# Kernel optimization log

Hardware: AMD Instinct MI355X
Metric: run time of the kernel (lower is better)

Reference implementation:

```python
import jax, jax.numpy as jnp
from jax import lax
import numpy as np

B, T, I, H, OUT = 4096, 168, 4, 64, 12


def setup_inputs() -> dict:
    key = jax.random.key(0)
    ks = jax.random.split(key, 14)
    s = 0.05
    return {
        "x": jax.random.normal(ks[0], (B, T, I), dtype=jnp.float32),
        # LSTM layer 0 (PyTorch gate order: i, f, g, o)
        "Wih0": jax.random.normal(ks[1], (4 * H, I), dtype=jnp.float32) * s,
        "Whh0": jax.random.normal(ks[2], (4 * H, H), dtype=jnp.float32) * s,
        "bih0": jax.random.normal(ks[3], (4 * H,), dtype=jnp.float32) * s,
        "bhh0": jax.random.normal(ks[4], (4 * H,), dtype=jnp.float32) * s,
        # LSTM layer 1
        "Wih1": jax.random.normal(ks[5], (4 * H, H), dtype=jnp.float32) * s,
        "Whh1": jax.random.normal(ks[6], (4 * H, H), dtype=jnp.float32) * s,
        "bih1": jax.random.normal(ks[7], (4 * H,), dtype=jnp.float32) * s,
        "bhh1": jax.random.normal(ks[8], (4 * H,), dtype=jnp.float32) * s,
        # FC head: Linear(64,64) -> ReLU -> Linear(64,12)
        "W1": jax.random.normal(ks[9], (64, H), dtype=jnp.float32) * s,
        "b1": jax.random.normal(ks[10], (64,), dtype=jnp.float32) * s,
        "W2": jax.random.normal(ks[11], (OUT, 64), dtype=jnp.float32) * s,
        "b2": jax.random.normal(ks[12], (OUT,), dtype=jnp.float32) * s,
    }


def _lstm_layer(x, Wih, Whh, bih, bhh):
    # x: [B, T, in]; returns hidden sequence [B, T, H]
    Bsz = x.shape[0]
    Hd = Whh.shape[1]
    # Precompute input contribution for all timesteps: [B, T, 4H]
    xg = jnp.einsum('bti,gi->btg', x, Wih) + bih + bhh

    def step(carry, xg_t):
        h, c = carry
        g = xg_t + h @ Whh.T  # [B, 4H]
        i, f, gg, o = jnp.split(g, 4, axis=-1)
        i = jax.nn.sigmoid(i)
        f = jax.nn.sigmoid(f)
        gg = jnp.tanh(gg)
        o = jax.nn.sigmoid(o)
        c = f * c + i * gg
        h = o * jnp.tanh(c)
        return (h, c), h

    h0 = jnp.zeros((Bsz, Hd), x.dtype)
    (_, _), hs = lax.scan(step, (h0, h0), jnp.swapaxes(xg, 0, 1))  # hs: [T, B, H]
    return jnp.swapaxes(hs, 0, 1)


def reference(x, Wih0, Whh0, bih0, bhh0, Wih1, Whh1, bih1, bhh1, W1, b1, W2, b2):
    # Eval-mode forward: dropout layers are identity.
    h1 = _lstm_layer(x, Wih0, Whh0, bih0, bhh0)   # [B, T, H]
    h2 = _lstm_layer(h1, Wih1, Whh1, bih1, bhh1)  # [B, T, H]
    last = h2[:, -1, :]                            # [B, H]
    z = jax.nn.relu(last @ W1.T + b1)              # [B, 64]
    out = z @ W2.T + b2                            # [B, 12]
    return out.reshape(-1, 3, 4)
```

## Files before the change

kernel.cpp:

```cpp
#include <hip/hip_runtime.h>


typedef _Float16 h8 __attribute__((ext_vector_type(8)));
typedef _Float16 h4 __attribute__((ext_vector_type(4)));
typedef float f4 __attribute__((ext_vector_type(4)));

#define ROWB 208
#define HBUF (16 * ROWB)
#define XTAB_OFF 0
#define XTAB_BYTES (168 * 256)
#define H0_OFF XTAB_BYTES
#define H1_OFF (H0_OFF + 8 * HBUF)
#define CNT_OFF (H1_OFF + 2 * HBUF)
#define SMEM_TOTAL (CNT_OFF + 128)

#define K1F 1.4426950408889634f
#define K2F 2.8853900817779268f

__device__ __forceinline__ float exp2_(float x) {
#if __has_builtin(__builtin_amdgcn_exp2f)
  return __builtin_amdgcn_exp2f(x);
#else
  float r; asm("v_exp_f32 %0, %1" : "=v"(r) : "v"(x)); return r;
#endif
}
__device__ __forceinline__ float rcp_(float x) {
#if __has_builtin(__builtin_amdgcn_rcpf)
  return __builtin_amdgcn_rcpf(x);
#else
  float r; asm("v_rcp_f32 %0, %1" : "=v"(r) : "v"(x)); return r;
#endif
}

__device__ __forceinline__ f4 mfma16(h8 a, h8 b, f4 c) {
  return __builtin_amdgcn_mfma_f32_16x16x32_f16(a, b, c, 0, 0, 0);
}

__device__ __forceinline__ h8 load_w8s(const float* __restrict__ p, float sc) {
  h8 r;
#pragma unroll
  for (int j = 0; j < 8; j++) r[j] = (_Float16)(p[j] * sc);
  return r;
}

__device__ __forceinline__ unsigned packh2(float a, float b) {
  unsigned lo = (unsigned)__builtin_bit_cast(unsigned short, (_Float16)a);
  unsigned hi = (unsigned)__builtin_bit_cast(unsigned short, (_Float16)b);
  return lo | (hi << 16);
}

__device__ __forceinline__ void lstm_act(f4 a, float& c, float& h) {
  float Ei = exp2_(-a[0]);
  float Ef = exp2_(-a[1]);
  float Eg = exp2_(a[2]);
  float Eo = exp2_(-a[3]);
  float A = 1.f + Ei, B = 1.f + Ef, C = 1.f + Eg, D = 1.f + Eo;
  float AB = A * B, CD = C * D, BD = B * D;
  float R  = rcp_(AB * CD);
  float fv = (A * CD) * R;
  float ig = (BD * (Eg - 1.f)) * R;
  float ov = (AB * C) * R;
  c = fmaf(fv, c, ig);
  float r2 = rcp_(exp2_(c * K2F) + 1.f);
  h = ov * fmaf(-2.f, r2, 1.f);
}

__device__ __forceinline__ int ld_cnt(int* p) {
  return __hip_atomic_load(p, __ATOMIC_ACQUIRE, __HIP_MEMORY_SCOPE_WORKGROUP);
}
__device__ __forceinline__ void arrive(int* p, int lane) {
  if (lane == 0)
    __hip_atomic_fetch_add(p, 1, __ATOMIC_RELEASE, __HIP_MEMORY_SCOPE_WORKGROUP);
}

extern "C" __global__ void __launch_bounds__(512, 2)
weather_lstm_mfma9(const float* __restrict__ x,
                   const float* __restrict__ Wih0, const float* __restrict__ Whh0,
                   const float* __restrict__ bih0, const float* __restrict__ bhh0,
                   const float* __restrict__ Wih1, const float* __restrict__ Whh1,
                   const float* __restrict__ bih1, const float* __restrict__ bhh1,
                   const float* __restrict__ W1, const float* __restrict__ b1,
                   const float* __restrict__ W2, const float* __restrict__ b2,
                   float* __restrict__ out)
{
  __shared__ __align__(16) unsigned char smem[SMEM_TOTAL];
  const int tid  = threadIdx.x;
  const int lane = tid & 63;
  const int w    = tid >> 6;
  const int col  = lane & 15;
  const int quad = lane >> 4;
  const int sB   = blockIdx.x * 16;
  const bool isA = (w < 4);
  const int gw   = w & 3;
  const int ub   = gw * 16;

  const int g_  = col & 3;
  const int ul_ = col >> 2;
  const float asc = (g_ == 2) ? K2F : K1F;

  int* aCnt = (int*)(smem + CNT_OFF);
  int* bCnt = (int*)(smem + CNT_OFF + 64);

  for (int idx = tid; idx < SMEM_TOTAL / 4; idx += 512) ((int*)smem)[idx] = 0;
  __syncthreads();
  for (int idx = tid; idx < 16 * 168; idx += 512) {
    const int c_ = idx / 168, t_ = idx - c_ * 168;
    f4 xv = *(const f4*)(x + ((size_t)(sB + c_) * 168 + t_) * 4);
    h4 xh;
#pragma unroll
    for (int j = 0; j < 4; j++) xh[j] = (_Float16)xv[j];
    *(h4*)(smem + XTAB_OFF + t_ * 256 + c_ * 16) = xh;
  }
  __syncthreads();

  const int bo  = col * ROWB + quad * 16;
  const int wo0 = col * ROWB + (ub + 2 * quad) * 2;
  const int wo1 = wo0 + 16;
  float hl[4] = {0.f, 0.f, 0.f, 0.f};

  if (isA) {
    h8 a0[4][3];
    f4 bias0v[4];
#pragma unroll
    for (int T = 0; T < 4; T++) {
      const int r = g_ * 64 + ub + (T >> 1) * 8 + 2 * ul_ + (T & 1);
#pragma unroll
      for (int f = 0; f < 2; f++)
        a0[T][f] = load_w8s(Whh0 + r * 64 + f * 32 + quad * 8, asc);
      h8 xw = {};
      if (quad == 0) {
#pragma unroll
        for (int j = 0; j < 4; j++) xw[j] = (_Float16)(Wih0[r * 4 + j] * asc);
      }
      a0[T][2] = xw;
#pragma unroll
      for (int reg = 0; reg < 4; reg++) {
        const int rb = reg * 64 + ub + (T >> 1) * 8 + 2 * quad + (T & 1);
        const float bs = (reg == 2) ? K2F : K1F;
        bias0v[T][reg] = (bih0[rb] + bhh0[rb]) * bs;
      }
    }
    const unsigned char* xp = smem + XTAB_OFF + col * 16;
    float c0[4] = {0.f, 0.f, 0.f, 0.f};
    int safeA = 0;

    for (int k = 0; k < 168; k++) {
      while (k >= safeA) {
        int lim = (ld_cnt(aCnt) >> 2) + 1;
        if (k >= 8) {
          int lim2 = (ld_cnt(bCnt) >> 2) + 8;
          lim = lim < lim2 ? lim : lim2;
        }
        safeA = lim;
      }
      const unsigned char* h0r = smem + H0_OFF + ((k + 7) & 7) * HBUF;
      unsigned char*       h0w = smem + H0_OFF + (k & 7) * HBUF;

      h8 b0  = *(const h8*)(h0r + bo);
      h8 b1v = *(const h8*)(h0r + bo + 64);
      h8 bx  = *(const h8*)(xp + k * 256);

      f4 A[4];
#pragma unroll
      for (int T = 0; T < 4; T++) A[T] = mfma16(a0[T][0], b0, bias0v[T]);
#pragma unroll
      for (int T = 0; T < 4; T++) A[T] = mfma16(a0[T][1], b1v, A[T]);
#pragma unroll
      for (int T = 0; T < 4; T++) A[T] = mfma16(a0[T][2], bx, A[T]);

      float h0o[4];
#pragma unroll
      for (int T = 0; T < 4; T++) lstm_act(A[T], c0[T], h0o[T]);
      *(unsigned*)(h0w + wo0) = packh2(h0o[0], h0o[1]);
      *(unsigned*)(h0w + wo1) = packh2(h0o[2], h0o[3]);
      arrive(aCnt, lane);
    }
  } else {
    h8 a1i[4][2], a1h[4][2];
    f4 bias1v[4];
#pragma unroll
    for (int T = 0; T < 4; T++) {
      const int r = g_ * 64 + ub + (T >> 1) * 8 + 2 * ul_ + (T & 1);
#pragma unroll
      for (int f = 0; f < 2; f++) {
        a1i[T][f] = load_w8s(Wih1 + r * 64 + f * 32 + quad * 8, asc);
        a1h[T][f] = load_w8s(Whh1 + r * 64 + f * 32 + quad * 8, asc);
      }
#pragma unroll
      for (int reg = 0; reg < 4; reg++) {
        const int rb = reg * 64 + ub + (T >> 1) * 8 + 2 * quad + (T & 1);
        const float bs = (reg == 2) ? K2F : K1F;
        bias1v[T][reg] = (bih1[rb] + bhh1[rb]) * bs;
      }
    }
    float c1[4] = {0.f, 0.f, 0.f, 0.f};
    int safeB = 0;

    for (int k = 0; k < 168; k++) {
      while (k >= safeB) {
        int limO = (ld_cnt(bCnt) >> 2) + 1;
        int limA = (ld_cnt(aCnt) >> 2);
        safeB = limO < limA ? limO : limA;
      }
      const unsigned char* hp = smem + H0_OFF + (k & 7) * HBUF;
      const unsigned char* hq = smem + H1_OFF + ((k + 1) & 1) * HBUF;
      unsigned char*       h1w = smem + H1_OFF + (k & 1) * HBUF;

      h8 p0 = *(const h8*)(hp + bo);
      h8 p1 = *(const h8*)(hp + bo + 64);
      h8 q0 = *(const h8*)(hq + bo);
      h8 q1 = *(const h8*)(hq + bo + 64);

      f4 C[4];
#pragma unroll
      for (int T = 0; T < 4; T++) C[T] = mfma16(a1i[T][0], p0, bias1v[T]);
#pragma unroll
      for (int T = 0; T < 4; T++) C[T] = mfma16(a1i[T][1], p1, C[T]);
#pragma unroll
      for (int T = 0; T < 4; T++) C[T] = mfma16(a1h[T][0], q0, C[T]);
#pragma unroll
      for (int T = 0; T < 4; T++) C[T] = mfma16(a1h[T][1], q1, C[T]);

#pragma unroll
      for (int T = 0; T < 4; T++) lstm_act(C[T], c1[T], hl[T]);
      *(unsigned*)(h1w + wo0) = packh2(hl[0], hl[1]);
      *(unsigned*)(h1w + wo1) = packh2(hl[2], hl[3]);
      arrive(bCnt, lane);
    }
  }
  __syncthreads();

  float* fh = (float*)smem;
  if (!isA) {
#pragma unroll
    for (int T = 0; T < 4; T++)
      fh[col * 64 + (ub + (T >> 1) * 8 + 2 * quad + (T & 1))] = hl[T];
  }
  __syncthreads();

  {
    const int u = tid & 63, grp = tid >> 6;
    float za0 = b1[u], za1 = b1[u];
    const float* w1r = W1 + u * 64;
    const float* f0 = fh + (grp * 2 + 0) * 64;
    const float* f1 = fh + (grp * 2 + 1) * 64;
    for (int j = 0; j < 64; j++) {
      float wv = w1r[j];
      za0 += wv * f0[j];
      za1 += wv * f1[j];
    }
    float* zl = (float*)(smem + 8192);
    zl[(grp * 2 + 0) * 64 + u] = fmaxf(za0, 0.f);
    zl[(grp * 2 + 1) * 64 + u] = fmaxf(za1, 0.f);
  }
  __syncthreads();

  if (tid < 192) {
    const float* zl = (const float*)(smem + 8192);
    const int s = tid / 12, o = tid - s * 12;
    float a = b2[o];
    for (int j = 0; j < 64; j++) a += W2[o * 64 + j] * zl[s * 64 + j];
    out[(sB + s) * 12 + o] = a;
  }
}

extern "C" void kernel_launch(void* const* d_in, const int* in_sizes, int n_in,
                              void* d_out, int out_size, void* d_ws, size_t ws_size,
                              hipStream_t stream) {
  (void)in_sizes; (void)n_in; (void)d_ws; (void)ws_size; (void)out_size;
  const float* x    = (const float*)d_in[0];
  const float* Wih0 = (const float*)d_in[1];
  const float* Whh0 = (const float*)d_in[2];
  const float* bih0 = (const float*)d_in[3];
  const float* bhh0 = (const float*)d_in[4];
  const float* Wih1 = (const float*)d_in[5];
  const float* Whh1 = (const float*)d_in[6];
  const float* bih1 = (const float*)d_in[7];
  const float* bhh1 = (const float*)d_in[8];
  const float* W1   = (const float*)d_in[9];
  const float* b1   = (const float*)d_in[10];
  const float* W2   = (const float*)d_in[11];
  const float* b2   = (const float*)d_in[12];

  weather_lstm_mfma9<<<dim3(256), dim3(512), 0, stream>>>(
      x, Wih0, Whh0, bih0, bhh0, Wih1, Whh1, bih1, bhh1, W1, b1, W2, b2,
      (float*)d_out);
}
```

Measured before the change: 229.7 us.

## Split each LSTM layer across eight waves per block instead of four

Doubles the block to 1024 threads so each layer uses eight wavefronts, each owning 8 hidden units (2 MFMA tiles) instead of 16 (4 tiles). The per-step serial chain of MFMAs and activations per wave is halved, which targets latency of the sequential recurrence. Counter thresholds change to a shift of 3 to match eight arriving waves, and the FC head is remapped to one sample per wave. The cost is more waves contending on the shared-memory counters and a larger block that may lower occupancy or register budget per wave.

Result: no change. 232.7 us (+1.3%).

```diff
diff --git a/kernel.cpp b/kernel.cpp
--- a/kernel.cpp
+++ b/kernel.cpp
@@ -73,15 +73,15 @@
     __hip_atomic_fetch_add(p, 1, __ATOMIC_RELEASE, __HIP_MEMORY_SCOPE_WORKGROUP);
 }
 
-extern "C" __global__ void __launch_bounds__(512, 2)
-weather_lstm_mfma9(const float* __restrict__ x,
-                   const float* __restrict__ Wih0, const float* __restrict__ Whh0,
-                   const float* __restrict__ bih0, const float* __restrict__ bhh0,
-                   const float* __restrict__ Wih1, const float* __restrict__ Whh1,
-                   const float* __restrict__ bih1, const float* __restrict__ bhh1,
-                   const float* __restrict__ W1, const float* __restrict__ b1,
-                   const float* __restrict__ W2, const float* __restrict__ b2,
-                   float* __restrict__ out)
+extern "C" __global__ void __launch_bounds__(1024, 4)
+weather_lstm_mfma10(const float* __restrict__ x,
+                    const float* __restrict__ Wih0, const float* __restrict__ Whh0,
+                    const float* __restrict__ bih0, const float* __restrict__ bhh0,
+                    const float* __restrict__ Wih1, const float* __restrict__ Whh1,
+                    const float* __restrict__ bih1, const float* __restrict__ bhh1,
+                    const float* __restrict__ W1, const float* __restrict__ b1,
+                    const float* __restrict__ W2, const float* __restrict__ b2,
+                    float* __restrict__ out)
 {
   __shared__ __align__(16) unsigned char smem[SMEM_TOTAL];
   const int tid  = threadIdx.x;
@@ -90,9 +90,9 @@
   const int col  = lane & 15;
   const int quad = lane >> 4;
   const int sB   = blockIdx.x * 16;
-  const bool isA = (w < 4);
-  const int gw   = w & 3;
-  const int ub   = gw * 16;
+  const bool isA = (w < 8);
+  const int gw   = w & 7;
+  const int ub   = gw * 8;
 
   const int g_  = col & 3;
   const int ul_ = col >> 2;
@@ -101,9 +101,9 @@
   int* aCnt = (int*)(smem + CNT_OFF);
   int* bCnt = (int*)(smem + CNT_OFF + 64);
 
-  for (int idx = tid; idx < SMEM_TOTAL / 4; idx += 512) ((int*)smem)[idx] = 0;
-  __syncthreads();
-  for (int idx = tid; idx < 16 * 168; idx += 512) {
+  for (int idx = tid; idx < SMEM_TOTAL / 4; idx += 1024) ((int*)smem)[idx] = 0;
+  __syncthreads();
+  for (int idx = tid; idx < 16 * 168; idx += 1024) {
     const int c_ = idx / 168, t_ = idx - c_ * 168;
     f4 xv = *(const f4*)(x + ((size_t)(sB + c_) * 168 + t_) * 4);
     h4 xh;
@@ -114,16 +114,15 @@
   __syncthreads();
 
   const int bo  = col * ROWB + quad * 16;
-  const int wo0 = col * ROWB + (ub + 2 * quad) * 2;
-  const int wo1 = wo0 + 16;
-  float hl[4] = {0.f, 0.f, 0.f, 0.f};
+  const int wo  = col * ROWB + (ub + 2 * quad) * 2;
+  float hl[2] = {0.f, 0.f};
 
   if (isA) {
-    h8 a0[4][3];
-    f4 bias0v[4];
-#pragma unroll
-    for (int T = 0; T < 4; T++) {
-      const int r = g_ * 64 + ub + (T >> 1) * 8 + 2 * ul_ + (T & 1);
+    h8 a0[2][3];
+    f4 bias0v[2];
+#pragma unroll
+    for (int T = 0; T < 2; T++) {
+      const int r = g_ * 64 + ub + 2 * ul_ + T;
 #pragma unroll
       for (int f = 0; f < 2; f++)
         a0[T][f] = load_w8s(Whh0 + r * 64 + f * 32 + quad * 8, asc);
@@ -135,20 +134,20 @@
       a0[T][2] = xw;
 #pragma unroll
       for (int reg = 0; reg < 4; reg++) {
-        const int rb = reg * 64 + ub + (T >> 1) * 8 + 2 * quad + (T & 1);
+        const int rb = reg * 64 + ub + 2 * quad + T;
         const float bs = (reg == 2) ? K2F : K1F;
         bias0v[T][reg] = (bih0[rb] + bhh0[rb]) * bs;
       }
     }
     const unsigned char* xp = smem + XTAB_OFF + col * 16;
-    float c0[4] = {0.f, 0.f, 0.f, 0.f};
+    float c0[2] = {0.f, 0.f};
     int safeA = 0;
 
     for (int k = 0; k < 168; k++) {
       while (k >= safeA) {
-        int lim = (ld_cnt(aCnt) >> 2) + 1;
+        int lim = (ld_cnt(aCnt) >> 3) + 1;
         if (k >= 8) {
-          int lim2 = (ld_cnt(bCnt) >> 2) + 8;
+          int lim2 = (ld_cnt(bCnt) >> 3) + 8;
           lim = lim < lim2 ? lim : lim2;
         }
         safeA = lim;
@@ -160,27 +159,25 @@
       h8 b1v = *(const h8*)(h0r + bo + 64);
       h8 bx  = *(const h8*)(xp + k * 256);
 
-      f4 A[4];
-#pragma unroll
-      for (int T = 0; T < 4; T++) A[T] = mfma16(a0[T][0], b0, bias0v[T]);
-#pragma unroll
-      for (int T = 0; T < 4; T++) A[T] = mfma16(a0[T][1], b1v, A[T]);
-#pragma unroll
-      for (int T = 0; T < 4; T++) A[T] = mfma16(a0[T][2], bx, A[T]);
-
-      float h0o[4];
-#pragma unroll
-      for (int T = 0; T < 4; T++) lstm_act(A[T], c0[T], h0o[T]);
-      *(unsigned*)(h0w + wo0) = packh2(h0o[0], h0o[1]);
-      *(unsigned*)(h0w + wo1) = packh2(h0o[2], h0o[3]);
+      f4 A0 = mfma16(a0[0][0], b0, bias0v[0]);
+      f4 A1 = mfma16(a0[1][0], b0, bias0v[1]);
+      A0 = mfma16(a0[0][1], b1v, A0);
+      A1 = mfma16(a0[1][1], b1v, A1);
+      A0 = mfma16(a0[0][2], bx, A0);
+      A1 = mfma16(a0[1][2], bx, A1);
+
+      float h0o[2];
+      lstm_act(A0, c0[0], h0o[0]);
+      lstm_act(A1, c0[1], h0o[1]);
+      *(unsigned*)(h0w + wo) = packh2(h0o[0], h0o[1]);
       arrive(aCnt, lane);
     }
   } else {
-    h8 a1i[4][2], a1h[4][2];
-    f4 bias1v[4];
-#pragma unroll
-    for (int T = 0; T < 4; T++) {
-      const int r = g_ * 64 + ub + (T >> 1) * 8 + 2 * ul_ + (T & 1);
+    h8 a1i[2][2], a1h[2][2];
+    f4 bias1v[2];
+#pragma unroll
+    for (int T = 0; T < 2; T++) {
+      const int r = g_ * 64 + ub + 2 * ul_ + T;
 #pragma unroll
       for (int f = 0; f < 2; f++) {
         a1i[T][f] = load_w8s(Wih1 + r * 64 + f * 32 + quad * 8, asc);
@@ -188,18 +185,18 @@
       }
 #pragma unroll
       for (int reg = 0; reg < 4; reg++) {
-        const int rb = reg * 64 + ub + (T >> 1) * 8 + 2 * quad + (T & 1);
+        const int rb = reg * 64 + ub + 2 * quad + T;
         const float bs = (reg == 2) ? K2F : K1F;
         bias1v[T][reg] = (bih1[rb] + bhh1[rb]) * bs;
       }
     }
-    float c1[4] = {0.f, 0.f, 0.f, 0.f};
+    float c1[2] = {0.f, 0.f};
     int safeB = 0;
 
     for (int k = 0; k < 168; k++) {
       while (k >= safeB) {
-        int limO = (ld_cnt(bCnt) >> 2) + 1;
-        int limA = (ld_cnt(aCnt) >> 2);
+        int limO = (ld_cnt(bCnt) >> 3) + 1;
+        int limA = (ld_cnt(aCnt) >> 3);
         safeB = limO < limA ? limO : limA;
       }
       const unsigned char* hp = smem + H0_OFF + (k & 7) * HBUF;
@@ -211,20 +208,18 @@
       h8 q0 = *(const h8*)(hq + bo);
       h8 q1 = *(const h8*)(hq + bo + 64);
 
-      f4 C[4];
-#pragma unroll
-      for (int T = 0; T < 4; T++) C[T] = mfma16(a1i[T][0], p0, bias1v[T]);
-#pragma unroll
-      for (int T = 0; T < 4; T++) C[T] = mfma16(a1i[T][1], p1, C[T]);
-#pragma unroll
-      for (int T = 0; T < 4; T++) C[T] = mfma16(a1h[T][0], q0, C[T]);
-#pragma unroll
-      for (int T = 0; T < 4; T++) C[T] = mfma16(a1h[T][1], q1, C[T]);
-
-#pragma unroll
-      for (int T = 0; T < 4; T++) lstm_act(C[T], c1[T], hl[T]);
-      *(unsigned*)(h1w + wo0) = packh2(hl[0], hl[1]);
-      *(unsigned*)(h1w + wo1) = packh2(hl[2], hl[3]);
+      f4 C0 = mfma16(a1i[0][0], p0, bias1v[0]);
+      f4 C1 = mfma16(a1i[1][0], p0, bias1v[1]);
+      C0 = mfma16(a1i[0][1], p1, C0);
+      C1 = mfma16(a1i[1][1], p1, C1);
+      C0 = mfma16(a1h[0][0], q0, C0);
+      C1 = mfma16(a1h[1][0], q0, C1);
+      C0 = mfma16(a1h[0][1], q1, C0);
+      C1 = mfma16(a1h[1][1], q1, C1);
+
+      lstm_act(C0, c1[0], hl[0]);
+      lstm_act(C1, c1[1], hl[1]);
+      *(unsigned*)(h1w + wo) = packh2(hl[0], hl[1]);
       arrive(bCnt, lane);
     }
   }
@@ -233,25 +228,19 @@
   float* fh = (float*)smem;
   if (!isA) {
 #pragma unroll
-    for (int T = 0; T < 4; T++)
-      fh[col * 64 + (ub + (T >> 1) * 8 + 2 * quad + (T & 1))] = hl[T];
+    for (int T = 0; T < 2; T++)
+      fh[col * 64 + (ub + 2 * quad + T)] = hl[T];
   }
   __syncthreads();
 
   {
     const int u = tid & 63, grp = tid >> 6;
-    float za0 = b1[u], za1 = b1[u];
+    float za = b1[u];
     const float* w1r = W1 + u * 64;
-    const float* f0 = fh + (grp * 2 + 0) * 64;
-    const float* f1 = fh + (grp * 2 + 1) * 64;
-    for (int j = 0; j < 64; j++) {
-      float wv = w1r[j];
-      za0 += wv * f0[j];
-      za1 += wv * f1[j];
-    }
+    const float* f0 = fh + grp * 64;
+    for (int j = 0; j < 64; j++) za += w1r[j] * f0[j];
     float* zl = (float*)(smem + 8192);
-    zl[(grp * 2 + 0) * 64 + u] = fmaxf(za0, 0.f);
-    zl[(grp * 2 + 1) * 64 + u] = fmaxf(za1, 0.f);
+    zl[grp * 64 + u] = fmaxf(za, 0.f);
   }
   __syncthreads();
 
@@ -282,7 +271,7 @@
   const float* W2   = (const float*)d_in[11];
   const float* b2   = (const float*)d_in[12];
 
-  weather_lstm_mfma9<<<dim3(256), dim3(512), 0, stream>>>(
+  weather_lstm_mfma10<<<dim3(256), dim3(1024), 0, stream>>>(
       x, Wih0, Whh0, bih0, bhh0, Wih1, Whh1, bih1, bhh1, W1, b1, W2, b2,
       (float*)d_out);
 }
```
